# Performance work log

Measured on AMD Instinct MI355X. Metric: run time of the kernel, lower is better.

The kernel has to match this reference:

```python
import jax, jax.numpy as jnp
import numpy as np

N_ITER = 5
NMF_EPS = 1e-20
IP_EPS = 1e-20

M, J, I, K = 2, 2000, 2049, 8  # channels == sources, frames, freq bins, NMF bases


def setup_inputs() -> dict:
    key = jax.random.key(0)
    k1, k2, k3 = jax.random.split(key, 3)
    X = jax.random.normal(k1, (M, J, I, 2), dtype=jnp.float32)
    lo = 1e-08
    T0 = jax.random.uniform(k2, (I, K, M), dtype=jnp.float32) * (1 - lo) + lo
    V0 = jax.random.uniform(k3, (K, J, M), dtype=jnp.float32) * (1 - lo) + lo
    return {"X": X, "T0": T0, "V0": V0}


def nmf_update(T, V, Y, eps):
    # T: (I,K), V: (K,J), Y: (I,J) complex
    P = jnp.abs(Y) ** 2                       # power spectrogram (I,J)
    R = T @ V                                  # low-rank model (I,J)
    T = T * jnp.sqrt(((P / (R * R)) @ V.T) / ((1.0 / R) @ V.T))
    T = jnp.maximum(T, eps)
    R = T @ V
    V = V * jnp.sqrt((T.T @ (P / (R * R))) / (T.T @ (1.0 / R)))
    V = jnp.maximum(V, eps)
    R = T @ V
    return T, V, R


def reference(X, T0, V0):
    Mc, Jc, Ic, _ = X.shape
    N = Mc
    # view_as_complex(X.permute(2,0,1,3)) -> (I, M, J) complex
    Xc = jnp.transpose(X[..., 0] + 1j * X[..., 1], (2, 0, 1)).astype(jnp.complex64)
    eye_M = jnp.eye(Mc, dtype=jnp.complex64)
    W = jnp.broadcast_to(eye_M, (Ic, N, Mc))   # (I, N, M)
    T, V = T0, V0

    def body(carry, _):
        W, T, V = carry
        Y = jnp.einsum('inm,imj->inj', W, Xc)  # (I, N, J)
        for n in range(N):
            Tn, Vn, Rn = nmf_update(T[:, :, n], V[:, :, n], Y[:, n, :], NMF_EPS)
            T = T.at[:, :, n].set(Tn)
            V = V.at[:, :, n].set(Vn)
            inv_Rn = 1.0 / (Rn + IP_EPS)                       # (I, J)
            Xw = Xc * jnp.sqrt(inv_Rn)[:, None, :]             # (I, M, J)
            D = jnp.einsum('imj,ikj->imk', Xw, jnp.conj(Xw)) / Jc  # (I, M, M)
            Dreg = D + IP_EPS * eye_M
            A = jnp.einsum('inm,imk->ink', W, Dreg)            # (I, M, M)
            e_n = jnp.broadcast_to(eye_M[:, n], (Ic, Mc))
            b = jnp.linalg.solve(A, e_n[..., None])[..., 0]    # (I, M)
            quad = jnp.einsum('im,imk,ik->i', jnp.conj(b), Dreg, b)
            denom = jnp.sqrt(jnp.real(quad) + IP_EPS)          # (I,)
            W = W.at[:, n, :].set(jnp.conj(b / denom[:, None]))
        return (W, T, V), None

    (W, T, V), _ = jax.lax.scan(body, (W, T, V), None, length=N_ITER)
    Y = jnp.einsum('inm,imj->inj', W, Xc)                      # (I, N, J)
    Yp = jnp.transpose(Y, (1, 2, 0))                           # (N, J, I)
    return jnp.stack([jnp.real(Yp), jnp.imag(Yp)], axis=-1)    # (N, J, I, 2)
```

## Files before the change

kernel.cpp:

```cpp
#include <hip/hip_runtime.h>
#include <hip/hip_bf16.h>

#define M_CH 2
#define J_F 2000
#define I_F 2049
#define K_B 8
#define N_IT 5
#define NMF_EPS 1e-20f
#define IP_EPS 1e-20f
#define JCH 100
#define JCHSZ 20
#define PJT 100
#define PJSZ 20

__device__ __forceinline__ int swz900(int orig) {
  int xcd = orig & 7, rest = orig >> 3;
  return (xcd < 4 ? xcd * 113 : 452 + (xcd - 4) * 112) + rest;
}

__global__ void k_init(const float* __restrict__ T0, const float* __restrict__ V0,
                       float* __restrict__ T, float* __restrict__ V, float* __restrict__ W) {
  int t = blockIdx.x * blockDim.x + threadIdx.x;
  int stride = gridDim.x * blockDim.x;
  for (int idx = t; idx < 2 * I_F * K_B; idx += stride) {
    int n = idx / (I_F * K_B);
    int r = idx % (I_F * K_B);
    int i = r / K_B, k = r % K_B;
    T[idx] = T0[(i * K_B + k) * M_CH + n];
  }
  for (int idx = t; idx < 2 * K_B * J_F; idx += stride) {
    int n = idx / (K_B * J_F);
    int r = idx % (K_B * J_F);
    int k = r / J_F, j = r % J_F;
    V[idx] = V0[(k * J_F + j) * M_CH + n];
  }
  for (int i = t; i < I_F; i += stride) {
    W[i * 8 + 0] = 1.f; W[i * 8 + 1] = 0.f; W[i * 8 + 2] = 0.f; W[i * 8 + 3] = 0.f;
    W[i * 8 + 4] = 0.f; W[i * 8 + 5] = 0.f; W[i * 8 + 6] = 1.f; W[i * 8 + 7] = 0.f;
  }
}

__global__ __launch_bounds__(256) void k_pack(const float2* __restrict__ X,
                                              float4* __restrict__ Xp) {
  const int i = blockIdx.x * 256 + threadIdx.x;
  if (i >= I_F) return;
  const int j0 = blockIdx.y * 8;
  const int jend = min(8, J_F - j0);
  for (int jj = 0; jj < jend; ++jj) {
    const int j = j0 + jj;
    float2 a = X[(size_t)j * I_F + i];
    float2 b = X[(size_t)(J_F + j) * I_F + i];
    Xp[(size_t)j * I_F + i] = make_float4(a.x, a.y, b.x, b.y);
  }
}

__device__ __forceinline__ float4 load_x(const float4* Xp, const float2* X,
                                         int pk, size_t j, int i) {
  if (pk) return Xp[j * I_F + i];
  float2 a = X[j * I_F + i];
  float2 b = X[(size_t)J_F * I_F + j * I_F + i];
  return make_float4(a.x, a.y, b.x, b.y);
}

template<int PK>
__global__ __launch_bounds__(256) void k_T_partial(const float4* __restrict__ Xp,
                                                   const float2* __restrict__ X,
                                                   const float* __restrict__ W,
                                                   const float* __restrict__ T,
                                                   const float* __restrict__ V,
                                                   float* __restrict__ Tpart) {
  const int w = swz900(blockIdx.x);
  const int yb = w / 9, xb = w % 9;
  __shared__ float Vl[2][K_B][PJSZ];
  const int tid = threadIdx.x;
  const int j0 = yb * PJSZ;
  for (int idx = tid; idx < 2 * K_B * PJSZ; idx += 256) {
    int n = idx / (K_B * PJSZ);
    int rr = idx % (K_B * PJSZ);
    int k = rr / PJSZ, jj = rr % PJSZ;
    Vl[n][k][jj] = V[((size_t)n * K_B + k) * J_F + j0 + jj];
  }
  __syncthreads();
  const int i = xb * 256 + tid;
  if (i >= I_F) return;
  float tr0[K_B], tr1[K_B];
#pragma unroll
  for (int k = 0; k < K_B; ++k) {
    tr0[k] = T[(size_t)i * 8 + k];
    tr1[k] = T[((size_t)I_F + i) * 8 + k];
  }
  const float4 w0 = ((const float4*)W)[i * 2];
  const float4 w1 = ((const float4*)W)[i * 2 + 1];
  float num0[K_B] = {}, den0[K_B] = {}, num1[K_B] = {}, den1[K_B] = {};
#pragma unroll 2
  for (int jj = 0; jj < PJSZ; ++jj) {
    float4 x = load_x(Xp, X, PK, (size_t)(j0 + jj), i);
    float yr = w0.x * x.x - w0.y * x.y + w0.z * x.z - w0.w * x.w;
    float yi = w0.x * x.y + w0.y * x.x + w0.z * x.w + w0.w * x.z;
    float p0 = yr * yr + yi * yi;
    float zr = w1.x * x.x - w1.y * x.y + w1.z * x.z - w1.w * x.w;
    float zi = w1.x * x.y + w1.y * x.x + w1.z * x.w + w1.w * x.z;
    float p1 = zr * zr + zi * zi;
    float R0 = 0.f, R1 = 0.f;
#pragma unroll
    for (int k = 0; k < K_B; ++k) {
      R0 += tr0[k] * Vl[0][k][jj];
      R1 += tr1[k] * Vl[1][k][jj];
    }
    float a0 = p0 / (R0 * R0), b0 = 1.0f / R0;
    float a1 = p1 / (R1 * R1), b1 = 1.0f / R1;
#pragma unroll
    for (int k = 0; k < K_B; ++k) {
      num0[k] += a0 * Vl[0][k][jj]; den0[k] += b0 * Vl[0][k][jj];
      num1[k] += a1 * Vl[1][k][jj]; den1[k] += b1 * Vl[1][k][jj];
    }
  }
  float* b0_ = Tpart + (((size_t)0 * PJT + yb) * I_F + i) * 16;
  float* b1_ = Tpart + (((size_t)1 * PJT + yb) * I_F + i) * 16;
  *(float4*)(b0_ + 0)  = make_float4(num0[0], num0[1], num0[2], num0[3]);
  *(float4*)(b0_ + 4)  = make_float4(num0[4], num0[5], num0[6], num0[7]);
  *(float4*)(b0_ + 8)  = make_float4(den0[0], den0[1], den0[2], den0[3]);
  *(float4*)(b0_ + 12) = make_float4(den0[4], den0[5], den0[6], den0[7]);
  *(float4*)(b1_ + 0)  = make_float4(num1[0], num1[1], num1[2], num1[3]);
  *(float4*)(b1_ + 4)  = make_float4(num1[4], num1[5], num1[6], num1[7]);
  *(float4*)(b1_ + 8)  = make_float4(den1[0], den1[1], den1[2], den1[3]);
  *(float4*)(b1_ + 12) = make_float4(den1[4], den1[5], den1[6], den1[7]);
}

__global__ __launch_bounds__(256) void k_t_finish(const float* __restrict__ Tpart,
                                                  float* __restrict__ T) {
  int t = blockIdx.x * 256 + threadIdx.x;
  if (t >= 2 * I_F * K_B) return;
  int n = t / (I_F * K_B);
  int r = t % (I_F * K_B);
  int i = r >> 3, k = r & 7;
  const float* p = Tpart + (((size_t)n * PJT) * I_F + i) * 16;
  const size_t S = (size_t)I_F * 16;
  float n0 = 0.f, n1 = 0.f, n2 = 0.f, n3 = 0.f;
  float d0 = 0.f, d1 = 0.f, d2 = 0.f, d3 = 0.f;
  for (int jt = 0; jt < PJT; jt += 4) {
    n0 += p[jt * S + k];       d0 += p[jt * S + 8 + k];
    n1 += p[(jt + 1) * S + k]; d1 += p[(jt + 1) * S + 8 + k];
    n2 += p[(jt + 2) * S + k]; d2 += p[(jt + 2) * S + 8 + k];
    n3 += p[(jt + 3) * S + k]; d3 += p[(jt + 3) * S + 8 + k];
  }
  float num = (n0 + n1) + (n2 + n3);
  float den = (d0 + d1) + (d2 + d3);
  float told = T[t];
  T[t] = fmaxf(told * sqrtf(num / den), NMF_EPS);
}

template<int PK>
__global__ __launch_bounds__(256) void k_v_update(const float4* __restrict__ Xp,
                                                  const float2* __restrict__ X,
                                                  const float* __restrict__ W,
                                                  const float* __restrict__ T,
                                                  float* __restrict__ V) {
  const int j = blockIdx.x;
  const int tid = threadIdx.x;
  float vold0[K_B], vold1[K_B];
#pragma unroll
  for (int k = 0; k < K_B; ++k) {
    vold0[k] = V[(size_t)k * J_F + j];
    vold1[k] = V[(size_t)(K_B + k) * J_F + j];
  }
  float num0[K_B] = {}, den0[K_B] = {}, num1[K_B] = {}, den1[K_B] = {};
  const float* T1 = T + (size_t)I_F * K_B;
  for (int i = tid; i < I_F; i += 256) {
    float4 x = load_x(Xp, X, PK, (size_t)j, i);
    const float4 wa = ((const float4*)W)[i * 2];
    const float4 wb = ((const float4*)W)[i * 2 + 1];
    float yr = wa.x * x.x - wa.y * x.y + wa.z * x.z - wa.w * x.w;
    float yi = wa.x * x.y + wa.y * x.x + wa.z * x.w + wa.w * x.z;
    float p0 = yr * yr + yi * yi;
    float zr = wb.x * x.x - wb.y * x.y + wb.z * x.z - wb.w * x.w;
    float zi = wb.x * x.y + wb.y * x.x + wb.z * x.w + wb.w * x.z;
    float p1 = zr * zr + zi * zi;
    const float4 ta = *(const float4*)&T[i * 8];
    const float4 tb = *(const float4*)&T[i * 8 + 4];
    const float4 tc = *(const float4*)&T1[i * 8];
    const float4 td = *(const float4*)&T1[i * 8 + 4];
    float t0[K_B] = {ta.x, ta.y, ta.z, ta.w, tb.x, tb.y, tb.z, tb.w};
    float t1[K_B] = {tc.x, tc.y, tc.z, tc.w, td.x, td.y, td.z, td.w};
    float R0 = 0.f, R1 = 0.f;
#pragma unroll
    for (int k = 0; k < K_B; ++k) { R0 += t0[k] * vold0[k]; R1 += t1[k] * vold1[k]; }
    float a0 = p0 / (R0 * R0), b0 = 1.0f / R0;
    float a1 = p1 / (R1 * R1), b1 = 1.0f / R1;
#pragma unroll
    for (int k = 0; k < K_B; ++k) {
      num0[k] += a0 * t0[k]; den0[k] += b0 * t0[k];
      num1[k] += a1 * t1[k]; den1[k] += b1 * t1[k];
    }
  }
  __shared__ float red[4][32];
  const int lane = tid & 63, wid = tid >> 6;
#pragma unroll
  for (int k = 0; k < K_B; ++k) {
    float a0 = num0[k], b0 = den0[k], a1 = num1[k], b1 = den1[k];
#pragma unroll
    for (int off = 32; off > 0; off >>= 1) {
      a0 += __shfl_xor(a0, off, 64);
      b0 += __shfl_xor(b0, off, 64);
      a1 += __shfl_xor(a1, off, 64);
      b1 += __shfl_xor(b1, off, 64);
    }
    if (lane == 0) {
      red[wid][k] = a0; red[wid][8 + k] = b0;
      red[wid][16 + k] = a1; red[wid][24 + k] = b1;
    }
  }
  __syncthreads();
  if (tid < 32) red[0][tid] = red[0][tid] + red[1][tid] + red[2][tid] + red[3][tid];
  __syncthreads();
  if (tid < 16) {
    int n = tid >> 3, k = tid & 7;
    float nu = red[0][n * 16 + k];
    float de = red[0][n * 16 + 8 + k];
    size_t idx = ((size_t)n * K_B + k) * J_F + j;
    float vo = V[idx];
    V[idx] = fmaxf(vo * sqrtf(nu / de), NMF_EPS);
  }
}

template<int PK>
__global__ __launch_bounds__(256) void k_d_partial(const float4* __restrict__ Xp,
                                                   const float2* __restrict__ X,
                                                   const float* __restrict__ T,
                                                   const float* __restrict__ V,
                                                   float* __restrict__ Dpart) {
  const int w = swz900(blockIdx.x);
  const int yb = w / 9, xb = w % 9;
  __shared__ float Vl[2][K_B][JCHSZ];
  const int tid = threadIdx.x;
  const int j0 = yb * JCHSZ;
  for (int idx = tid; idx < 2 * K_B * JCHSZ; idx += 256) {
    int n = idx / (K_B * JCHSZ);
    int rr = idx % (K_B * JCHSZ);
    int k = rr / JCHSZ, jj = rr % JCHSZ;
    Vl[n][k][jj] = V[((size_t)n * K_B + k) * J_F + j0 + jj];
  }
  __syncthreads();
  const int i = xb * 256 + tid;
  if (i >= I_F) return;
  float tr0[K_B], tr1[K_B];
#pragma unroll
  for (int k = 0; k < K_B; ++k) {
    tr0[k] = T[(size_t)i * K_B + k];
    tr1[k] = T[((size_t)I_F + i) * K_B + k];
  }
  float a00 = 0.f, a11 = 0.f, a01r = 0.f, a01i = 0.f;
  float b00 = 0.f, b11 = 0.f, b01r = 0.f, b01i = 0.f;
#pragma unroll 2
  for (int jj = 0; jj < JCHSZ; ++jj) {
    float4 x = load_x(Xp, X, PK, (size_t)(j0 + jj), i);
    float R0 = 0.f, R1 = 0.f;
#pragma unroll
    for (int k = 0; k < K_B; ++k) {
      R0 += tr0[k] * Vl[0][k][jj];
      R1 += tr1[k] * Vl[1][k][jj];
    }
    float wv0 = 1.0f / (R0 + IP_EPS);
    float wv1 = 1.0f / (R1 + IP_EPS);
    float p00 = x.x * x.x + x.y * x.y;
    float p11 = x.z * x.z + x.w * x.w;
    float pr = x.x * x.z + x.y * x.w;
    float pi = x.y * x.z - x.x * x.w;
    a00 += wv0 * p00; a11 += wv0 * p11; a01r += wv0 * pr; a01i += wv0 * pi;
    b00 += wv1 * p00; b11 += wv1 * p11; b01r += wv1 * pr; b01i += wv1 * pi;
  }
  ((float4*)Dpart)[((size_t)0 * JCH + yb) * I_F + i] = make_float4(a00, a11, a01r, a01i);
  ((float4*)Dpart)[((size_t)1 * JCH + yb) * I_F + i] = make_float4(b00, b11, b01r, b01i);
}

__global__ __launch_bounds__(256) void k_d_solve(const float* __restrict__ Dpart,
                                                 float* __restrict__ W) {
  const int g = blockIdx.x * 256 + threadIdx.x;
  const int i = g >> 2;
  const int part = g & 3;
  if (i >= I_F) return;
  float4 wa = ((const float4*)W)[i * 2];
  float4 wb = ((const float4*)W)[i * 2 + 1];
  float w00r = wa.x, w00i = wa.y, w01r = wa.z, w01i = wa.w;
  float w10r = wb.x, w10i = wb.y, w11r = wb.z, w11i = wb.w;
  const float invJ = 1.0f / (float)J_F;
#pragma unroll
  for (int n = 0; n < 2; ++n) {
    const float4* dp = (const float4*)Dpart + (size_t)n * JCH * I_F + i;
    float d00 = 0.f, d11 = 0.f, d01r = 0.f, d01i = 0.f;
    for (int c = part * 25; c < part * 25 + 25; ++c) {
      float4 e = dp[(size_t)c * I_F];
      d00 += e.x; d11 += e.y; d01r += e.z; d01i += e.w;
    }
#pragma unroll
    for (int off = 1; off < 4; off <<= 1) {
      d00 += __shfl_xor(d00, off, 64);
      d11 += __shfl_xor(d11, off, 64);
      d01r += __shfl_xor(d01r, off, 64);
      d01i += __shfl_xor(d01i, off, 64);
    }
    d00 = d00 * invJ + IP_EPS;
    d11 = d11 * invJ + IP_EPS;
    d01r *= invJ; d01i *= invJ;
    float A00r = w00r * d00 + (w01r * d01r + w01i * d01i);
    float A00i = w00i * d00 + (w01i * d01r - w01r * d01i);
    float A01r = (w00r * d01r - w00i * d01i) + w01r * d11;
    float A01i = (w00r * d01i + w00i * d01r) + w01i * d11;
    float A10r = w10r * d00 + (w11r * d01r + w11i * d01i);
    float A10i = w10i * d00 + (w11i * d01r - w11r * d01i);
    float A11r = (w10r * d01r - w10i * d01i) + w11r * d11;
    float A11i = (w10r * d01i + w10i * d01r) + w11i * d11;
    float detr = (A00r * A11r - A00i * A11i) - (A01r * A10r - A01i * A10i);
    float deti = (A00r * A11i + A00i * A11r) - (A01r * A10i + A01i * A10r);
    float idet = 1.0f / (detr * detr + deti * deti);
    float n0r, n0i, n1r, n1i;
    if (n == 0) { n0r = A11r; n0i = A11i; n1r = -A10r; n1i = -A10i; }
    else        { n0r = -A01r; n0i = -A01i; n1r = A00r; n1i = A00i; }
    float b0r = (n0r * detr + n0i * deti) * idet;
    float b0i = (n0i * detr - n0r * deti) * idet;
    float b1r = (n1r * detr + n1i * deti) * idet;
    float b1i = (n1i * detr - n1r * deti) * idet;
    float cr = d01r * b1r - d01i * b1i;
    float ci = d01r * b1i + d01i * b1r;
    float quad = d00 * (b0r * b0r + b0i * b0i) + d11 * (b1r * b1r + b1i * b1i)
               + 2.0f * (b0r * cr + b0i * ci);
    float s = 1.0f / sqrtf(quad + IP_EPS);
    if (n == 0) { w00r = b0r * s; w00i = -b0i * s; w01r = b1r * s; w01i = -b1i * s; }
    else        { w10r = b0r * s; w10i = -b0i * s; w11r = b1r * s; w11i = -b1i * s; }
  }
  if (part == 0) {
    ((float4*)W)[i * 2]     = make_float4(w00r, w00i, w01r, w01i);
    ((float4*)W)[i * 2 + 1] = make_float4(w10r, w10i, w11r, w11i);
  }
}

template<int PK>
__global__ __launch_bounds__(256) void k_final(const float4* __restrict__ Xp,
                                               const float2* __restrict__ X,
                                               const float* __restrict__ W,
                                               float2* __restrict__ out) {
  const int i = blockIdx.x * 256 + threadIdx.x;
  if (i >= I_F) return;
  const float4 wa = ((const float4*)W)[i * 2];
  const float4 wb = ((const float4*)W)[i * 2 + 1];
  const int j0 = blockIdx.y * 8;
  const int jend = min(8, J_F - j0);
  for (int jj = 0; jj < jend; ++jj) {
    const int j = j0 + jj;
    float4 x = load_x(Xp, X, PK, (size_t)j, i);
    float y0r = wa.x * x.x - wa.y * x.y + wa.z * x.z - wa.w * x.w;
    float y0i = wa.x * x.y + wa.y * x.x + wa.z * x.w + wa.w * x.z;
    out[(size_t)j * I_F + i] = make_float2(y0r, y0i);
    float y1r = wb.x * x.x - wb.y * x.y + wb.z * x.z - wb.w * x.w;
    float y1i = wb.x * x.y + wb.y * x.x + wb.z * x.w + wb.w * x.z;
    out[(size_t)(J_F + j) * I_F + i] = make_float2(y1r, y1i);
  }
}

extern "C" void kernel_launch(void* const* d_in, const int* in_sizes, int n_in,
                              void* d_out, int out_size, void* d_ws, size_t ws_size,
                              hipStream_t stream) {
  const float2* X = (const float2*)d_in[0];
  const float* T0 = (const float*)d_in[1];
  const float* V0 = (const float*)d_in[2];
  char* ws = (char*)d_ws;
  size_t off = 0;
  auto alloc = [&](size_t bytes) -> void* {
    void* p = ws + off;
    off = (off + bytes + 255) & ~(size_t)255;
    return p;
  };
  float* W = (float*)alloc((size_t)I_F * 8 * 4);
  float* T = (float*)alloc((size_t)2 * I_F * K_B * 4);
  float* V = (float*)alloc((size_t)2 * K_B * J_F * 4);
  float* Scr = (float*)alloc((size_t)2 * PJT * I_F * 16 * 4);
  float* Tpart = Scr;
  float* Dpart = Scr;
  size_t off_no_pack = off;
  float4* Xp = (float4*)alloc((size_t)J_F * I_F * 16);
  const bool packed = (off <= ws_size);
  if (!packed) off = off_no_pack;

  k_init<<<128, 256, 0, stream>>>(T0, V0, T, V, W);
  if (packed) {
    k_pack<<<dim3(9, 250), 256, 0, stream>>>(X, Xp);
    for (int it = 0; it < N_IT; ++it) {
      k_T_partial<1><<<900, 256, 0, stream>>>(Xp, X, W, T, V, Tpart);
      k_t_finish<<<129, 256, 0, stream>>>(Tpart, T);
      k_v_update<1><<<J_F, 256, 0, stream>>>(Xp, X, W, T, V);
      k_d_partial<1><<<900, 256, 0, stream>>>(Xp, X, T, V, Dpart);
      k_d_solve<<<33, 256, 0, stream>>>(Dpart, W);
    }
    k_final<1><<<dim3(9, 250), 256, 0, stream>>>(Xp, X, W, (float2*)d_out);
  } else {
    for (int it = 0; it < N_IT; ++it) {
      k_T_partial<0><<<900, 256, 0, stream>>>(nullptr, X, W, T, V, Tpart);
      k_t_finish<<<129, 256, 0, stream>>>(Tpart, T);
      k_v_update<0><<<J_F, 256, 0, stream>>>(nullptr, X, W, T, V);
      k_d_partial<0><<<900, 256, 0, stream>>>(nullptr, X, T, V, Dpart);
      k_d_solve<<<33, 256, 0, stream>>>(Dpart, W);
    }
    k_final<0><<<dim3(9, 250), 256, 0, stream>>>(nullptr, X, W, (float2*)d_out);
  }
}
```

Baseline: 493.3 us.

## Double J-tiles for T and D partial kernels and split finish reduction

Templates the partial-reduction kernels on the number of frame tiles and uses 200 tiles (1800 blocks) instead of 100 when the workspace allows. The aim is more blocks in flight per CU for the memory-bound streaming over X. k_t_finish now splits each element's reduction across four lanes combined with shuffles, so the larger partial buffer is summed with more parallelism. In exchange the partial buffers double in size, adding write and read traffic.

```diff
diff --git a/kernel.cpp b/kernel.cpp
--- a/kernel.cpp
+++ b/kernel.cpp
@@ -8,14 +8,12 @@
 #define N_IT 5
 #define NMF_EPS 1e-20f
 #define IP_EPS 1e-20f
-#define JCH 100
-#define JCHSZ 20
-#define PJT 100
-#define PJSZ 20
-
-__device__ __forceinline__ int swz900(int orig) {
+
+template<int NB>
+__device__ __forceinline__ int swz(int orig) {
+  constexpr int q = NB / 8, r = NB % 8;
   int xcd = orig & 7, rest = orig >> 3;
-  return (xcd < 4 ? xcd * 113 : 452 + (xcd - 4) * 112) + rest;
+  return (xcd < r ? xcd * (q + 1) : r * (q + 1) + (xcd - r) * q) + rest;
 }
 
 __global__ void k_init(const float* __restrict__ T0, const float* __restrict__ V0,
@@ -62,22 +60,23 @@
   return make_float4(a.x, a.y, b.x, b.y);
 }
 
-template<int PK>
+template<int PK, int TILES>
 __global__ __launch_bounds__(256) void k_T_partial(const float4* __restrict__ Xp,
                                                    const float2* __restrict__ X,
                                                    const float* __restrict__ W,
                                                    const float* __restrict__ T,
                                                    const float* __restrict__ V,
                                                    float* __restrict__ Tpart) {
-  const int w = swz900(blockIdx.x);
+  constexpr int TSZ = J_F / TILES;
+  const int w = swz<9 * TILES>(blockIdx.x);
   const int yb = w / 9, xb = w % 9;
-  __shared__ float Vl[2][K_B][PJSZ];
+  __shared__ float Vl[2][K_B][TSZ];
   const int tid = threadIdx.x;
-  const int j0 = yb * PJSZ;
-  for (int idx = tid; idx < 2 * K_B * PJSZ; idx += 256) {
-    int n = idx / (K_B * PJSZ);
-    int rr = idx % (K_B * PJSZ);
-    int k = rr / PJSZ, jj = rr % PJSZ;
+  const int j0 = yb * TSZ;
+  for (int idx = tid; idx < 2 * K_B * TSZ; idx += 256) {
+    int n = idx / (K_B * TSZ);
+    int rr = idx % (K_B * TSZ);
+    int k = rr / TSZ, jj = rr % TSZ;
     Vl[n][k][jj] = V[((size_t)n * K_B + k) * J_F + j0 + jj];
   }
   __syncthreads();
@@ -93,7 +92,7 @@
   const float4 w1 = ((const float4*)W)[i * 2 + 1];
   float num0[K_B] = {}, den0[K_B] = {}, num1[K_B] = {}, den1[K_B] = {};
 #pragma unroll 2
-  for (int jj = 0; jj < PJSZ; ++jj) {
+  for (int jj = 0; jj < TSZ; ++jj) {
     float4 x = load_x(Xp, X, PK, (size_t)(j0 + jj), i);
     float yr = w0.x * x.x - w0.y * x.y + w0.z * x.z - w0.w * x.w;
     float yi = w0.x * x.y + w0.y * x.x + w0.z * x.w + w0.w * x.z;
@@ -115,8 +114,8 @@
       num1[k] += a1 * Vl[1][k][jj]; den1[k] += b1 * Vl[1][k][jj];
     }
   }
-  float* b0_ = Tpart + (((size_t)0 * PJT + yb) * I_F + i) * 16;
-  float* b1_ = Tpart + (((size_t)1 * PJT + yb) * I_F + i) * 16;
+  float* b0_ = Tpart + (((size_t)0 * TILES + yb) * I_F + i) * 16;
+  float* b1_ = Tpart + (((size_t)1 * TILES + yb) * I_F + i) * 16;
   *(float4*)(b0_ + 0)  = make_float4(num0[0], num0[1], num0[2], num0[3]);
   *(float4*)(b0_ + 4)  = make_float4(num0[4], num0[5], num0[6], num0[7]);
   *(float4*)(b0_ + 8)  = make_float4(den0[0], den0[1], den0[2], den0[3]);
@@ -127,27 +126,33 @@
   *(float4*)(b1_ + 12) = make_float4(den1[4], den1[5], den1[6], den1[7]);
 }
 
+template<int TILES>
 __global__ __launch_bounds__(256) void k_t_finish(const float* __restrict__ Tpart,
                                                   float* __restrict__ T) {
-  int t = blockIdx.x * 256 + threadIdx.x;
-  if (t >= 2 * I_F * K_B) return;
-  int n = t / (I_F * K_B);
-  int r = t % (I_F * K_B);
+  int g = blockIdx.x * 256 + threadIdx.x;
+  int e = g >> 2, part = g & 3;
+  if (e >= 2 * I_F * K_B) return;
+  int n = e / (I_F * K_B);
+  int r = e % (I_F * K_B);
   int i = r >> 3, k = r & 7;
-  const float* p = Tpart + (((size_t)n * PJT) * I_F + i) * 16;
   const size_t S = (size_t)I_F * 16;
-  float n0 = 0.f, n1 = 0.f, n2 = 0.f, n3 = 0.f;
-  float d0 = 0.f, d1 = 0.f, d2 = 0.f, d3 = 0.f;
-  for (int jt = 0; jt < PJT; jt += 4) {
-    n0 += p[jt * S + k];       d0 += p[jt * S + 8 + k];
-    n1 += p[(jt + 1) * S + k]; d1 += p[(jt + 1) * S + 8 + k];
-    n2 += p[(jt + 2) * S + k]; d2 += p[(jt + 2) * S + 8 + k];
-    n3 += p[(jt + 3) * S + k]; d3 += p[(jt + 3) * S + 8 + k];
-  }
-  float num = (n0 + n1) + (n2 + n3);
-  float den = (d0 + d1) + (d2 + d3);
-  float told = T[t];
-  T[t] = fmaxf(told * sqrtf(num / den), NMF_EPS);
+  const float* p = Tpart + ((size_t)n * TILES) * S + (size_t)i * 16;
+  constexpr int per = TILES / 4;
+  int jt = part * per;
+  const int jend = jt + per;
+  float n0 = 0.f, n1 = 0.f, d0 = 0.f, d1 = 0.f;
+  for (; jt + 1 < jend; jt += 2) {
+    n0 += p[(size_t)jt * S + k];         d0 += p[(size_t)jt * S + 8 + k];
+    n1 += p[(size_t)(jt + 1) * S + k];   d1 += p[(size_t)(jt + 1) * S + 8 + k];
+  }
+  if (jt < jend) { n0 += p[(size_t)jt * S + k]; d0 += p[(size_t)jt * S + 8 + k]; }
+  float num = n0 + n1, den = d0 + d1;
+  num += __shfl_xor(num, 1, 64); den += __shfl_xor(den, 1, 64);
+  num += __shfl_xor(num, 2, 64); den += __shfl_xor(den, 2, 64);
+  if (part == 0) {
+    float told = T[e];
+    T[e] = fmaxf(told * sqrtf(num / den), NMF_EPS);
+  }
 }
 
 template<int PK>
@@ -223,21 +228,22 @@
   }
 }
 
-template<int PK>
+template<int PK, int TILES>
 __global__ __launch_bounds__(256) void k_d_partial(const float4* __restrict__ Xp,
                                                    const float2* __restrict__ X,
                                                    const float* __restrict__ T,
                                                    const float* __restrict__ V,
                                                    float* __restrict__ Dpart) {
-  const int w = swz900(blockIdx.x);
+  constexpr int TSZ = J_F / TILES;
+  const int w = swz<9 * TILES>(blockIdx.x);
   const int yb = w / 9, xb = w % 9;
-  __shared__ float Vl[2][K_B][JCHSZ];
+  __shared__ float Vl[2][K_B][TSZ];
   const int tid = threadIdx.x;
-  const int j0 = yb * JCHSZ;
-  for (int idx = tid; idx < 2 * K_B * JCHSZ; idx += 256) {
-    int n = idx / (K_B * JCHSZ);
-    int rr = idx % (K_B * JCHSZ);
-    int k = rr / JCHSZ, jj = rr % JCHSZ;
+  const int j0 = yb * TSZ;
+  for (int idx = tid; idx < 2 * K_B * TSZ; idx += 256) {
+    int n = idx / (K_B * TSZ);
+    int rr = idx % (K_B * TSZ);
+    int k = rr / TSZ, jj = rr % TSZ;
     Vl[n][k][jj] = V[((size_t)n * K_B + k) * J_F + j0 + jj];
   }
   __syncthreads();
@@ -252,7 +258,7 @@
   float a00 = 0.f, a11 = 0.f, a01r = 0.f, a01i = 0.f;
   float b00 = 0.f, b11 = 0.f, b01r = 0.f, b01i = 0.f;
 #pragma unroll 2
-  for (int jj = 0; jj < JCHSZ; ++jj) {
+  for (int jj = 0; jj < TSZ; ++jj) {
     float4 x = load_x(Xp, X, PK, (size_t)(j0 + jj), i);
     float R0 = 0.f, R1 = 0.f;
 #pragma unroll
@@ -269,16 +275,18 @@
     a00 += wv0 * p00; a11 += wv0 * p11; a01r += wv0 * pr; a01i += wv0 * pi;
     b00 += wv1 * p00; b11 += wv1 * p11; b01r += wv1 * pr; b01i += wv1 * pi;
   }
-  ((float4*)Dpart)[((size_t)0 * JCH + yb) * I_F + i] = make_float4(a00, a11, a01r, a01i);
-  ((float4*)Dpart)[((size_t)1 * JCH + yb) * I_F + i] = make_float4(b00, b11, b01r, b01i);
-}
-
+  ((float4*)Dpart)[((size_t)0 * TILES + yb) * I_F + i] = make_float4(a00, a11, a01r, a01i);
+  ((float4*)Dpart)[((size_t)1 * TILES + yb) * I_F + i] = make_float4(b00, b11, b01r, b01i);
+}
+
+template<int TILES>
 __global__ __launch_bounds__(256) void k_d_solve(const float* __restrict__ Dpart,
                                                  float* __restrict__ W) {
   const int g = blockIdx.x * 256 + threadIdx.x;
   const int i = g >> 2;
   const int part = g & 3;
   if (i >= I_F) return;
+  constexpr int per = TILES / 4;
   float4 wa = ((const float4*)W)[i * 2];
   float4 wb = ((const float4*)W)[i * 2 + 1];
   float w00r = wa.x, w00i = wa.y, w01r = wa.z, w01i = wa.w;
@@ -286,9 +294,10 @@
   const float invJ = 1.0f / (float)J_F;
 #pragma unroll
   for (int n = 0; n < 2; ++n) {
-    const float4* dp = (const float4*)Dpart + (size_t)n * JCH * I_F + i;
+    const float4* dp = (const float4*)Dpart + (size_t)n * TILES * I_F + i;
     float d00 = 0.f, d11 = 0.f, d01r = 0.f, d01i = 0.f;
-    for (int c = part * 25; c < part * 25 + 25; ++c) {
+#pragma unroll 2
+    for (int c = part * per; c < part * per + per; ++c) {
       float4 e = dp[(size_t)c * I_F];
       d00 += e.x; d11 += e.y; d01r += e.z; d01i += e.w;
     }
@@ -373,32 +382,46 @@
   float* W = (float*)alloc((size_t)I_F * 8 * 4);
   float* T = (float*)alloc((size_t)2 * I_F * K_B * 4);
   float* V = (float*)alloc((size_t)2 * K_B * J_F * 4);
-  float* Scr = (float*)alloc((size_t)2 * PJT * I_F * 16 * 4);
+  const size_t scr200 = (size_t)2 * 200 * I_F * 16 * 4;
+  const size_t scr100 = (size_t)2 * 100 * I_F * 16 * 4;
+  const size_t xp_sz = (size_t)J_F * I_F * 16;
+  int cfg;
+  if (off + scr200 + 256 + xp_sz <= ws_size) cfg = 0;
+  else if (off + scr100 + 256 + xp_sz <= ws_size) cfg = 1;
+  else cfg = 2;
+  float* Scr = (float*)alloc(cfg == 0 ? scr200 : scr100);
+  float4* Xp = (cfg <= 1) ? (float4*)alloc(xp_sz) : nullptr;
   float* Tpart = Scr;
   float* Dpart = Scr;
-  size_t off_no_pack = off;
-  float4* Xp = (float4*)alloc((size_t)J_F * I_F * 16);
-  const bool packed = (off <= ws_size);
-  if (!packed) off = off_no_pack;
 
   k_init<<<128, 256, 0, stream>>>(T0, V0, T, V, W);
-  if (packed) {
+  if (cfg == 0) {
     k_pack<<<dim3(9, 250), 256, 0, stream>>>(X, Xp);
     for (int it = 0; it < N_IT; ++it) {
-      k_T_partial<1><<<900, 256, 0, stream>>>(Xp, X, W, T, V, Tpart);
-      k_t_finish<<<129, 256, 0, stream>>>(Tpart, T);
+      k_T_partial<1, 200><<<1800, 256, 0, stream>>>(Xp, X, W, T, V, Tpart);
+      k_t_finish<200><<<513, 256, 0, stream>>>(Tpart, T);
       k_v_update<1><<<J_F, 256, 0, stream>>>(Xp, X, W, T, V);
-      k_d_partial<1><<<900, 256, 0, stream>>>(Xp, X, T, V, Dpart);
-      k_d_solve<<<33, 256, 0, stream>>>(Dpart, W);
+      k_d_partial<1, 200><<<1800, 256, 0, stream>>>(Xp, X, T, V, Dpart);
+      k_d_solve<200><<<33, 256, 0, stream>>>(Dpart, W);
+    }
+    k_final<1><<<dim3(9, 250), 256, 0, stream>>>(Xp, X, W, (float2*)d_out);
+  } else if (cfg == 1) {
+    k_pack<<<dim3(9, 250), 256, 0, stream>>>(X, Xp);
+    for (int it = 0; it < N_IT; ++it) {
+      k_T_partial<1, 100><<<900, 256, 0, stream>>>(Xp, X, W, T, V, Tpart);
+      k_t_finish<100><<<513, 256, 0, stream>>>(Tpart, T);
+      k_v_update<1><<<J_F, 256, 0, stream>>>(Xp, X, W, T, V);
+      k_d_partial<1, 100><<<900, 256, 0, stream>>>(Xp, X, T, V, Dpart);
+      k_d_solve<100><<<33, 256, 0, stream>>>(Dpart, W);
     }
     k_final<1><<<dim3(9, 250), 256, 0, stream>>>(Xp, X, W, (float2*)d_out);
   } else {
     for (int it = 0; it < N_IT; ++it) {
-      k_T_partial<0><<<900, 256, 0, stream>>>(nullptr, X, W, T, V, Tpart);
-      k_t_finish<<<129, 256, 0, stream>>>(Tpart, T);
+      k_T_partial<0, 100><<<900, 256, 0, stream>>>(nullptr, X, W, T, V, Tpart);
+      k_t_finish<100><<<513, 256, 0, stream>>>(Tpart, T);
       k_v_update<0><<<J_F, 256, 0, stream>>>(nullptr, X, W, T, V);
-      k_d_partial<0><<<900, 256, 0, stream>>>(nullptr, X, T, V, Dpart);
-      k_d_solve<<<33, 256, 0, stream>>>(Dpart, W);
+      k_d_partial<0, 100><<<900, 256, 0, stream>>>(nullptr, X, T, V, Dpart);
+      k_d_solve<100><<<33, 256, 0, stream>>>(Dpart, W);
     }
     k_final<0><<<dim3(9, 250), 256, 0, stream>>>(nullptr, X, W, (float2*)d_out);
   }
```

Result: slower. 576.2 us (+16.8%).

## Add frequency-major packed copy of X and fuse T/D reductions per row

Applied to the files above, without the earlier changes.

Adds a transposed packed copy of X (frequency-major, j contiguous) built once via a shared-memory transpose. The T update and the demixing-matrix statistics are each rewritten as one block per frequency bin that loops over frames and reduces in-block. This replaces the partial-sum kernels and their finish and solve kernels, removing the scratch round trips and two launches per iteration. It costs a second full copy of X in workspace plus an extra transpose pass, and V is now read straight from global memory instead of staged in LDS.

```diff
diff --git a/kernel.cpp b/kernel.cpp
--- a/kernel.cpp
+++ b/kernel.cpp
@@ -8,15 +8,6 @@
 #define N_IT 5
 #define NMF_EPS 1e-20f
 #define IP_EPS 1e-20f
-#define JCH 100
-#define JCHSZ 20
-#define PJT 100
-#define PJSZ 20
-
-__device__ __forceinline__ int swz900(int orig) {
-  int xcd = orig & 7, rest = orig >> 3;
-  return (xcd < 4 ? xcd * 113 : 452 + (xcd - 4) * 112) + rest;
-}
 
 __global__ void k_init(const float* __restrict__ T0, const float* __restrict__ V0,
                        float* __restrict__ T, float* __restrict__ V, float* __restrict__ W) {
@@ -54,6 +45,31 @@
   }
 }
 
+__global__ __launch_bounds__(256) void k_packT(const float2* __restrict__ X,
+                                               float4* __restrict__ Xpt) {
+  __shared__ float4 Tl[32][33];
+  const int tid = threadIdx.x;
+  const int i0 = blockIdx.x * 32, j0 = blockIdx.y * 32;
+  const int la = tid & 31, su = tid >> 5;
+#pragma unroll
+  for (int p = 0; p < 4; ++p) {
+    int jj = su + p * 8;
+    int i = i0 + la, j = j0 + jj;
+    if (i < I_F && j < J_F) {
+      float2 a = X[(size_t)j * I_F + i];
+      float2 b = X[(size_t)(J_F + j) * I_F + i];
+      Tl[la][jj] = make_float4(a.x, a.y, b.x, b.y);
+    }
+  }
+  __syncthreads();
+#pragma unroll
+  for (int p = 0; p < 4; ++p) {
+    int ii = su + p * 8;
+    int i = i0 + ii, j = j0 + la;
+    if (i < I_F && j < J_F) Xpt[(size_t)i * J_F + j] = Tl[ii][la];
+  }
+}
+
 __device__ __forceinline__ float4 load_x(const float4* Xp, const float2* X,
                                          int pk, size_t j, int i) {
   if (pk) return Xp[j * I_F + i];
@@ -62,27 +78,22 @@
   return make_float4(a.x, a.y, b.x, b.y);
 }
 
+__device__ __forceinline__ float4 load_xt(const float4* Xpt, const float2* X,
+                                          int pk, int i, int j) {
+  if (pk) return Xpt[(size_t)i * J_F + j];
+  float2 a = X[(size_t)j * I_F + i];
+  float2 b = X[(size_t)(J_F + j) * I_F + i];
+  return make_float4(a.x, a.y, b.x, b.y);
+}
+
 template<int PK>
-__global__ __launch_bounds__(256) void k_T_partial(const float4* __restrict__ Xp,
-                                                   const float2* __restrict__ X,
-                                                   const float* __restrict__ W,
-                                                   const float* __restrict__ T,
-                                                   const float* __restrict__ V,
-                                                   float* __restrict__ Tpart) {
-  const int w = swz900(blockIdx.x);
-  const int yb = w / 9, xb = w % 9;
-  __shared__ float Vl[2][K_B][PJSZ];
+__global__ __launch_bounds__(256) void k_T_rows(const float4* __restrict__ Xpt,
+                                                const float2* __restrict__ X,
+                                                const float* __restrict__ W,
+                                                float* __restrict__ T,
+                                                const float* __restrict__ V) {
+  const int i = blockIdx.x;
   const int tid = threadIdx.x;
-  const int j0 = yb * PJSZ;
-  for (int idx = tid; idx < 2 * K_B * PJSZ; idx += 256) {
-    int n = idx / (K_B * PJSZ);
-    int rr = idx % (K_B * PJSZ);
-    int k = rr / PJSZ, jj = rr % PJSZ;
-    Vl[n][k][jj] = V[((size_t)n * K_B + k) * J_F + j0 + jj];
-  }
-  __syncthreads();
-  const int i = xb * 256 + tid;
-  if (i >= I_F) return;
   float tr0[K_B], tr1[K_B];
 #pragma unroll
   for (int k = 0; k < K_B; ++k) {
@@ -92,62 +103,57 @@
   const float4 w0 = ((const float4*)W)[i * 2];
   const float4 w1 = ((const float4*)W)[i * 2 + 1];
   float num0[K_B] = {}, den0[K_B] = {}, num1[K_B] = {}, den1[K_B] = {};
-#pragma unroll 2
-  for (int jj = 0; jj < PJSZ; ++jj) {
-    float4 x = load_x(Xp, X, PK, (size_t)(j0 + jj), i);
+  for (int j = tid; j < J_F; j += 256) {
+    float4 x = load_xt(Xpt, X, PK, i, j);
     float yr = w0.x * x.x - w0.y * x.y + w0.z * x.z - w0.w * x.w;
     float yi = w0.x * x.y + w0.y * x.x + w0.z * x.w + w0.w * x.z;
     float p0 = yr * yr + yi * yi;
     float zr = w1.x * x.x - w1.y * x.y + w1.z * x.z - w1.w * x.w;
     float zi = w1.x * x.y + w1.y * x.x + w1.z * x.w + w1.w * x.z;
     float p1 = zr * zr + zi * zi;
+    float v0[K_B], v1[K_B];
     float R0 = 0.f, R1 = 0.f;
 #pragma unroll
     for (int k = 0; k < K_B; ++k) {
-      R0 += tr0[k] * Vl[0][k][jj];
-      R1 += tr1[k] * Vl[1][k][jj];
+      v0[k] = V[(size_t)k * J_F + j];           R0 += tr0[k] * v0[k];
+      v1[k] = V[(size_t)(K_B + k) * J_F + j];   R1 += tr1[k] * v1[k];
     }
     float a0 = p0 / (R0 * R0), b0 = 1.0f / R0;
     float a1 = p1 / (R1 * R1), b1 = 1.0f / R1;
 #pragma unroll
     for (int k = 0; k < K_B; ++k) {
-      num0[k] += a0 * Vl[0][k][jj]; den0[k] += b0 * Vl[0][k][jj];
-      num1[k] += a1 * Vl[1][k][jj]; den1[k] += b1 * Vl[1][k][jj];
-    }
-  }
-  float* b0_ = Tpart + (((size_t)0 * PJT + yb) * I_F + i) * 16;
-  float* b1_ = Tpart + (((size_t)1 * PJT + yb) * I_F + i) * 16;
-  *(float4*)(b0_ + 0)  = make_float4(num0[0], num0[1], num0[2], num0[3]);
-  *(float4*)(b0_ + 4)  = make_float4(num0[4], num0[5], num0[6], num0[7]);
-  *(float4*)(b0_ + 8)  = make_float4(den0[0], den0[1], den0[2], den0[3]);
-  *(float4*)(b0_ + 12) = make_float4(den0[4], den0[5], den0[6], den0[7]);
-  *(float4*)(b1_ + 0)  = make_float4(num1[0], num1[1], num1[2], num1[3]);
-  *(float4*)(b1_ + 4)  = make_float4(num1[4], num1[5], num1[6], num1[7]);
-  *(float4*)(b1_ + 8)  = make_float4(den1[0], den1[1], den1[2], den1[3]);
-  *(float4*)(b1_ + 12) = make_float4(den1[4], den1[5], den1[6], den1[7]);
-}
-
-__global__ __launch_bounds__(256) void k_t_finish(const float* __restrict__ Tpart,
-                                                  float* __restrict__ T) {
-  int t = blockIdx.x * 256 + threadIdx.x;
-  if (t >= 2 * I_F * K_B) return;
-  int n = t / (I_F * K_B);
-  int r = t % (I_F * K_B);
-  int i = r >> 3, k = r & 7;
-  const float* p = Tpart + (((size_t)n * PJT) * I_F + i) * 16;
-  const size_t S = (size_t)I_F * 16;
-  float n0 = 0.f, n1 = 0.f, n2 = 0.f, n3 = 0.f;
-  float d0 = 0.f, d1 = 0.f, d2 = 0.f, d3 = 0.f;
-  for (int jt = 0; jt < PJT; jt += 4) {
-    n0 += p[jt * S + k];       d0 += p[jt * S + 8 + k];
-    n1 += p[(jt + 1) * S + k]; d1 += p[(jt + 1) * S + 8 + k];
-    n2 += p[(jt + 2) * S + k]; d2 += p[(jt + 2) * S + 8 + k];
-    n3 += p[(jt + 3) * S + k]; d3 += p[(jt + 3) * S + 8 + k];
-  }
-  float num = (n0 + n1) + (n2 + n3);
-  float den = (d0 + d1) + (d2 + d3);
-  float told = T[t];
-  T[t] = fmaxf(told * sqrtf(num / den), NMF_EPS);
+      num0[k] += a0 * v0[k]; den0[k] += b0 * v0[k];
+      num1[k] += a1 * v1[k]; den1[k] += b1 * v1[k];
+    }
+  }
+  __shared__ float red[4][32];
+  const int lane = tid & 63, wid = tid >> 6;
+#pragma unroll
+  for (int k = 0; k < K_B; ++k) {
+    float a0 = num0[k], b0 = den0[k], a1 = num1[k], b1 = den1[k];
+#pragma unroll
+    for (int off = 32; off > 0; off >>= 1) {
+      a0 += __shfl_xor(a0, off, 64);
+      b0 += __shfl_xor(b0, off, 64);
+      a1 += __shfl_xor(a1, off, 64);
+      b1 += __shfl_xor(b1, off, 64);
+    }
+    if (lane == 0) {
+      red[wid][k] = a0; red[wid][8 + k] = b0;
+      red[wid][16 + k] = a1; red[wid][24 + k] = b1;
+    }
+  }
+  __syncthreads();
+  if (tid < 32) red[0][tid] = red[0][tid] + red[1][tid] + red[2][tid] + red[3][tid];
+  __syncthreads();
+  if (tid < 16) {
+    int n = tid >> 3, k = tid & 7;
+    float nu = red[0][n * 16 + k];
+    float de = red[0][n * 16 + 8 + k];
+    size_t idx = ((size_t)n * I_F + i) * 8 + k;
+    float told = T[idx];
+    T[idx] = fmaxf(told * sqrtf(nu / de), NMF_EPS);
+  }
 }
 
 template<int PK>
@@ -224,41 +230,27 @@
 }
 
 template<int PK>
-__global__ __launch_bounds__(256) void k_d_partial(const float4* __restrict__ Xp,
-                                                   const float2* __restrict__ X,
-                                                   const float* __restrict__ T,
-                                                   const float* __restrict__ V,
-                                                   float* __restrict__ Dpart) {
-  const int w = swz900(blockIdx.x);
-  const int yb = w / 9, xb = w % 9;
-  __shared__ float Vl[2][K_B][JCHSZ];
+__global__ __launch_bounds__(256) void k_d_rows(const float4* __restrict__ Xpt,
+                                                const float2* __restrict__ X,
+                                                const float* __restrict__ T,
+                                                const float* __restrict__ V,
+                                                float* __restrict__ W) {
+  const int i = blockIdx.x;
   const int tid = threadIdx.x;
-  const int j0 = yb * JCHSZ;
-  for (int idx = tid; idx < 2 * K_B * JCHSZ; idx += 256) {
-    int n = idx / (K_B * JCHSZ);
-    int rr = idx % (K_B * JCHSZ);
-    int k = rr / JCHSZ, jj = rr % JCHSZ;
-    Vl[n][k][jj] = V[((size_t)n * K_B + k) * J_F + j0 + jj];
-  }
-  __syncthreads();
-  const int i = xb * 256 + tid;
-  if (i >= I_F) return;
   float tr0[K_B], tr1[K_B];
 #pragma unroll
   for (int k = 0; k < K_B; ++k) {
     tr0[k] = T[(size_t)i * K_B + k];
     tr1[k] = T[((size_t)I_F + i) * K_B + k];
   }
-  float a00 = 0.f, a11 = 0.f, a01r = 0.f, a01i = 0.f;
-  float b00 = 0.f, b11 = 0.f, b01r = 0.f, b01i = 0.f;
-#pragma unroll 2
-  for (int jj = 0; jj < JCHSZ; ++jj) {
-    float4 x = load_x(Xp, X, PK, (size_t)(j0 + jj), i);
+  float acc[8] = {};
+  for (int j = tid; j < J_F; j += 256) {
+    float4 x = load_xt(Xpt, X, PK, i, j);
     float R0 = 0.f, R1 = 0.f;
 #pragma unroll
     for (int k = 0; k < K_B; ++k) {
-      R0 += tr0[k] * Vl[0][k][jj];
-      R1 += tr1[k] * Vl[1][k][jj];
+      R0 += tr0[k] * V[(size_t)k * J_F + j];
+      R1 += tr1[k] * V[(size_t)(K_B + k) * J_F + j];
     }
     float wv0 = 1.0f / (R0 + IP_EPS);
     float wv1 = 1.0f / (R1 + IP_EPS);
@@ -266,69 +258,59 @@
     float p11 = x.z * x.z + x.w * x.w;
     float pr = x.x * x.z + x.y * x.w;
     float pi = x.y * x.z - x.x * x.w;
-    a00 += wv0 * p00; a11 += wv0 * p11; a01r += wv0 * pr; a01i += wv0 * pi;
-    b00 += wv1 * p00; b11 += wv1 * p11; b01r += wv1 * pr; b01i += wv1 * pi;
-  }
-  ((float4*)Dpart)[((size_t)0 * JCH + yb) * I_F + i] = make_float4(a00, a11, a01r, a01i);
-  ((float4*)Dpart)[((size_t)1 * JCH + yb) * I_F + i] = make_float4(b00, b11, b01r, b01i);
-}
-
-__global__ __launch_bounds__(256) void k_d_solve(const float* __restrict__ Dpart,
-                                                 float* __restrict__ W) {
-  const int g = blockIdx.x * 256 + threadIdx.x;
-  const int i = g >> 2;
-  const int part = g & 3;
-  if (i >= I_F) return;
-  float4 wa = ((const float4*)W)[i * 2];
-  float4 wb = ((const float4*)W)[i * 2 + 1];
-  float w00r = wa.x, w00i = wa.y, w01r = wa.z, w01i = wa.w;
-  float w10r = wb.x, w10i = wb.y, w11r = wb.z, w11i = wb.w;
-  const float invJ = 1.0f / (float)J_F;
-#pragma unroll
-  for (int n = 0; n < 2; ++n) {
-    const float4* dp = (const float4*)Dpart + (size_t)n * JCH * I_F + i;
-    float d00 = 0.f, d11 = 0.f, d01r = 0.f, d01i = 0.f;
-    for (int c = part * 25; c < part * 25 + 25; ++c) {
-      float4 e = dp[(size_t)c * I_F];
-      d00 += e.x; d11 += e.y; d01r += e.z; d01i += e.w;
-    }
-#pragma unroll
-    for (int off = 1; off < 4; off <<= 1) {
-      d00 += __shfl_xor(d00, off, 64);
-      d11 += __shfl_xor(d11, off, 64);
-      d01r += __shfl_xor(d01r, off, 64);
-      d01i += __shfl_xor(d01i, off, 64);
-    }
-    d00 = d00 * invJ + IP_EPS;
-    d11 = d11 * invJ + IP_EPS;
-    d01r *= invJ; d01i *= invJ;
-    float A00r = w00r * d00 + (w01r * d01r + w01i * d01i);
-    float A00i = w00i * d00 + (w01i * d01r - w01r * d01i);
-    float A01r = (w00r * d01r - w00i * d01i) + w01r * d11;
-    float A01i = (w00r * d01i + w00i * d01r) + w01i * d11;
-    float A10r = w10r * d00 + (w11r * d01r + w11i * d01i);
-    float A10i = w10i * d00 + (w11i * d01r - w11r * d01i);
-    float A11r = (w10r * d01r - w10i * d01i) + w11r * d11;
-    float A11i = (w10r * d01i + w10i * d01r) + w11i * d11;
-    float detr = (A00r * A11r - A00i * A11i) - (A01r * A10r - A01i * A10i);
-    float deti = (A00r * A11i + A00i * A11r) - (A01r * A10i + A01i * A10r);
-    float idet = 1.0f / (detr * detr + deti * deti);
-    float n0r, n0i, n1r, n1i;
-    if (n == 0) { n0r = A11r; n0i = A11i; n1r = -A10r; n1i = -A10i; }
-    else        { n0r = -A01r; n0i = -A01i; n1r = A00r; n1i = A00i; }
-    float b0r = (n0r * detr + n0i * deti) * idet;
-    float b0i = (n0i * detr - n0r * deti) * idet;
-    float b1r = (n1r * detr + n1i * deti) * idet;
-    float b1i = (n1i * detr - n1r * deti) * idet;
-    float cr = d01r * b1r - d01i * b1i;
-    float ci = d01r * b1i + d01i * b1r;
-    float quad = d00 * (b0r * b0r + b0i * b0i) + d11 * (b1r * b1r + b1i * b1i)
-               + 2.0f * (b0r * cr + b0i * ci);
-    float s = 1.0f / sqrtf(quad + IP_EPS);
-    if (n == 0) { w00r = b0r * s; w00i = -b0i * s; w01r = b1r * s; w01i = -b1i * s; }
-    else        { w10r = b0r * s; w10i = -b0i * s; w11r = b1r * s; w11i = -b1i * s; }
-  }
-  if (part == 0) {
+    acc[0] += wv0 * p00; acc[1] += wv0 * p11; acc[2] += wv0 * pr; acc[3] += wv0 * pi;
+    acc[4] += wv1 * p00; acc[5] += wv1 * p11; acc[6] += wv1 * pr; acc[7] += wv1 * pi;
+  }
+  __shared__ float red[4][8];
+  const int lane = tid & 63, wid = tid >> 6;
+#pragma unroll
+  for (int v = 0; v < 8; ++v) {
+    float a = acc[v];
+#pragma unroll
+    for (int off = 32; off > 0; off >>= 1) a += __shfl_xor(a, off, 64);
+    if (lane == 0) red[wid][v] = a;
+  }
+  __syncthreads();
+  if (tid < 8) red[0][tid] = red[0][tid] + red[1][tid] + red[2][tid] + red[3][tid];
+  __syncthreads();
+  if (tid == 0) {
+    float4 wa = ((const float4*)W)[i * 2];
+    float4 wb = ((const float4*)W)[i * 2 + 1];
+    float w00r = wa.x, w00i = wa.y, w01r = wa.z, w01i = wa.w;
+    float w10r = wb.x, w10i = wb.y, w11r = wb.z, w11i = wb.w;
+    const float invJ = 1.0f / (float)J_F;
+#pragma unroll
+    for (int n = 0; n < 2; ++n) {
+      float d00 = red[0][n * 4 + 0] * invJ + IP_EPS;
+      float d11 = red[0][n * 4 + 1] * invJ + IP_EPS;
+      float d01r = red[0][n * 4 + 2] * invJ;
+      float d01i = red[0][n * 4 + 3] * invJ;
+      float A00r = w00r * d00 + (w01r * d01r + w01i * d01i);
+      float A00i = w00i * d00 + (w01i * d01r - w01r * d01i);
+      float A01r = (w00r * d01r - w00i * d01i) + w01r * d11;
+      float A01i = (w00r * d01i + w00i * d01r) + w01i * d11;
+      float A10r = w10r * d00 + (w11r * d01r + w11i * d01i);
+      float A10i = w10i * d00 + (w11i * d01r - w11r * d01i);
+      float A11r = (w10r * d01r - w10i * d01i) + w11r * d11;
+      float A11i = (w10r * d01i + w10i * d01r) + w11i * d11;
+      float detr = (A00r * A11r - A00i * A11i) - (A01r * A10r - A01i * A10i);
+      float deti = (A00r * A11i + A00i * A11r) - (A01r * A10i + A01i * A10r);
+      float idet = 1.0f / (detr * detr + deti * deti);
+      float n0r, n0i, n1r, n1i;
+      if (n == 0) { n0r = A11r; n0i = A11i; n1r = -A10r; n1i = -A10i; }
+      else        { n0r = -A01r; n0i = -A01i; n1r = A00r; n1i = A00i; }
+      float b0r = (n0r * detr + n0i * deti) * idet;
+      float b0i = (n0i * detr - n0r * deti) * idet;
+      float b1r = (n1r * detr + n1i * deti) * idet;
+      float b1i = (n1i * detr - n1r * deti) * idet;
+      float cr = d01r * b1r - d01i * b1i;
+      float ci = d01r * b1i + d01i * b1r;
+      float quad = d00 * (b0r * b0r + b0i * b0i) + d11 * (b1r * b1r + b1i * b1i)
+                 + 2.0f * (b0r * cr + b0i * ci);
+      float s = 1.0f / sqrtf(quad + IP_EPS);
+      if (n == 0) { w00r = b0r * s; w00i = -b0i * s; w01r = b1r * s; w01i = -b1i * s; }
+      else        { w10r = b0r * s; w10i = -b0i * s; w11r = b1r * s; w11i = -b1i * s; }
+    }
     ((float4*)W)[i * 2]     = make_float4(w00r, w00i, w01r, w01i);
     ((float4*)W)[i * 2 + 1] = make_float4(w10r, w10i, w11r, w11i);
   }
@@ -373,32 +355,36 @@
   float* W = (float*)alloc((size_t)I_F * 8 * 4);
   float* T = (float*)alloc((size_t)2 * I_F * K_B * 4);
   float* V = (float*)alloc((size_t)2 * K_B * J_F * 4);
-  float* Scr = (float*)alloc((size_t)2 * PJT * I_F * 16 * 4);
-  float* Tpart = Scr;
-  float* Dpart = Scr;
-  size_t off_no_pack = off;
-  float4* Xp = (float4*)alloc((size_t)J_F * I_F * 16);
-  const bool packed = (off <= ws_size);
-  if (!packed) off = off_no_pack;
+  const size_t x_sz = (size_t)J_F * I_F * 16;
+  float4* Xpt = nullptr;
+  float4* Xp = nullptr;
+  if (off + x_sz <= ws_size) Xpt = (float4*)alloc(x_sz);
+  if (Xpt && off + x_sz <= ws_size) Xp = (float4*)alloc(x_sz);
+  const int pkt = Xpt != nullptr, pkj = Xp != nullptr;
 
   k_init<<<128, 256, 0, stream>>>(T0, V0, T, V, W);
-  if (packed) {
-    k_pack<<<dim3(9, 250), 256, 0, stream>>>(X, Xp);
+  if (pkt) k_packT<<<dim3(65, 63), 256, 0, stream>>>(X, Xpt);
+  if (pkj) k_pack<<<dim3(9, 250), 256, 0, stream>>>(X, Xp);
+
+  if (pkt && pkj) {
     for (int it = 0; it < N_IT; ++it) {
-      k_T_partial<1><<<900, 256, 0, stream>>>(Xp, X, W, T, V, Tpart);
-      k_t_finish<<<129, 256, 0, stream>>>(Tpart, T);
+      k_T_rows<1><<<I_F, 256, 0, stream>>>(Xpt, X, W, T, V);
       k_v_update<1><<<J_F, 256, 0, stream>>>(Xp, X, W, T, V);
-      k_d_partial<1><<<900, 256, 0, stream>>>(Xp, X, T, V, Dpart);
-      k_d_solve<<<33, 256, 0, stream>>>(Dpart, W);
+      k_d_rows<1><<<I_F, 256, 0, stream>>>(Xpt, X, T, V, W);
     }
     k_final<1><<<dim3(9, 250), 256, 0, stream>>>(Xp, X, W, (float2*)d_out);
+  } else if (pkt) {
+    for (int it = 0; it < N_IT; ++it) {
+      k_T_rows<1><<<I_F, 256, 0, stream>>>(Xpt, X, W, T, V);
+      k_v_update<0><<<J_F, 256, 0, stream>>>(nullptr, X, W, T, V);
+      k_d_rows<1><<<I_F, 256, 0, stream>>>(Xpt, X, T, V, W);
+    }
+    k_final<0><<<dim3(9, 250), 256, 0, stream>>>(nullptr, X, W, (float2*)d_out);
   } else {
     for (int it = 0; it < N_IT; ++it) {
-      k_T_partial<0><<<900, 256, 0, stream>>>(nullptr, X, W, T, V, Tpart);
-      k_t_finish<<<129, 256, 0, stream>>>(Tpart, T);
+      k_T_rows<0><<<I_F, 256, 0, stream>>>(nullptr, X, W, T, V);
       k_v_update<0><<<J_F, 256, 0, stream>>>(nullptr, X, W, T, V);
-      k_d_partial<0><<<900, 256, 0, stream>>>(nullptr, X, T, V, Dpart);
-      k_d_solve<<<33, 256, 0, stream>>>(Dpart, W);
+      k_d_rows<0><<<I_F, 256, 0, stream>>>(nullptr, X, T, V, W);
     }
     k_final<0><<<dim3(9, 250), 256, 0, stream>>>(nullptr, X, W, (float2*)d_out);
   }
```

New measurement: 490.2 us. No clear change (-0.6%).
